# Performance work log

Hardware: AMD Instinct MI355X
Metric: run time of the kernel (lower is better)

Reference implementation:

```python
import jax, jax.numpy as jnp
import numpy as np

UP_RATIO = 2
DOWN_RATIO = 2
K = 12  # hard-coded filter size assumed by the fused kernel


def kaiser_sinc_filter1d(cutoff, half_width, kernel_size):
    # Exact replica of BigVGAN's kaiser_sinc_filter1d (even kernel branch).
    half_size = kernel_size // 2
    delta_f = 4.0 * half_width
    A = 2.285 * (half_size - 1) * np.pi * delta_f + 7.95
    if A > 50.0:
        beta = 0.1102 * (A - 8.7)
    elif A >= 21.0:
        beta = 0.5842 * (A - 21.0) ** 0.4 + 0.07886 * (A - 21.0)
    else:
        beta = 0.0
    window = np.kaiser(kernel_size, beta)  # symmetric, == torch.kaiser_window(periodic=False)
    time = np.arange(-half_size, half_size) + 0.5  # even kernel size
    filt = 2.0 * cutoff * window * np.sinc(2.0 * cutoff * time)
    filt = filt / filt.sum()
    return filt.astype(np.float32)


def setup_inputs() -> dict:
    key = jax.random.key(0)
    k1, k2, k3 = jax.random.split(key, 3)
    B, C, T = 16, 512, 8192
    x = jax.random.normal(k1, (B, C, T), dtype=jnp.float32)
    # log-scale SnakeBeta parameters (alpha_logscale=True -> params stored in log space)
    alpha = jax.random.normal(k2, (C,), dtype=jnp.float32) * 0.1
    beta = jax.random.normal(k3, (C,), dtype=jnp.float32) * 0.1
    up_filter = jnp.asarray(kaiser_sinc_filter1d(0.5 / UP_RATIO, 0.6 / UP_RATIO, K))
    down_filter = jnp.asarray(kaiser_sinc_filter1d(0.5 / DOWN_RATIO, 0.6 / DOWN_RATIO, K))
    return {"x": x, "up_filter": up_filter, "down_filter": down_filter,
            "alpha": alpha, "beta": beta}


def _depthwise_conv(x, filt, stride=1, lhs_dilation=1, pad=(0, 0)):
    # x: (B, C, T); shared 1-tap-bank depthwise conv: fold channels into batch.
    B, C, T = x.shape
    xr = x.reshape(B * C, 1, T)
    w = filt.reshape(1, 1, -1)
    out = jax.lax.conv_general_dilated(
        xr, w, window_strides=(stride,), padding=[pad],
        lhs_dilation=(lhs_dilation,),
        dimension_numbers=("NCH", "OIH", "NCH"))
    return out.reshape(B, C, -1)


def reference(x, up_filter, down_filter, alpha, beta):
    B, C, T = x.shape
    # ---- UpSample1d(ratio=2, kernel_size=12): replicate pad + conv_transpose ----
    pad = K // UP_RATIO - 1                              # 5
    pad_left = pad * UP_RATIO + (K - UP_RATIO) // 2      # 15
    pad_right = pad * UP_RATIO + (K - UP_RATIO + 1) // 2  # 15
    xp = jnp.pad(x, ((0, 0), (0, 0), (pad, pad)), mode="edge")
    # conv_transpose1d(stride=s) == lhs-dilated conv with flipped kernel, full padding
    up = UP_RATIO * _depthwise_conv(xp, up_filter[::-1],
                                    lhs_dilation=UP_RATIO, pad=(K - 1, K - 1))
    up = up[..., pad_left: up.shape[-1] - pad_right]      # (B, C, 2T)
    # ---- SnakeBeta activation (log-scale alpha/beta) ----
    a = jnp.exp(alpha)[None, :, None]
    b = jnp.exp(beta)[None, :, None]
    act = up + (1.0 / (b + 1e-9)) * jnp.sin(up * a) ** 2
    # ---- DownSample1d: replicate-padded lowpass FIR, stride 2 ----
    dl = K // 2 - 1   # 5 (even kernel)
    dr = K // 2       # 6
    actp = jnp.pad(act, ((0, 0), (0, 0), (dl, dr)), mode="edge")
    out = _depthwise_conv(actp, down_filter, stride=DOWN_RATIO)  # (B, C, T)
    return out
```

## Files before the change

### kernel.cpp

```cpp
#include <hip/hip_runtime.h>


#define T_LEN 8192
#define C_CH  512
#define B_N   16
#define W     8
#define BLOCK 256

__global__ __launch_bounds__(BLOCK) void act1d_kernel(
    const float* __restrict__ x,
    const float* __restrict__ uf_g,
    const float* __restrict__ df_g,
    const float* __restrict__ alpha,
    const float* __restrict__ beta,
    float* __restrict__ out)
{
    const int T = T_LEN;
    const int bid = blockIdx.x;
    const int row = bid >> 2;
    const int chunk = bid & 3;
    const int c = row & (C_CH - 1);
    const int nb = chunk * (BLOCK * W) + (int)threadIdx.x * W;
    const long rowoff = (long)row * T;
    const float* xrow = x + rowoff;

    float uf[12], df[12];
#pragma unroll
    for (int k = 0; k < 12; ++k) { uf[k] = 2.0f * uf_g[k]; df[k] = df_g[k]; }

    const float ea   = __expf(alpha[c]);
    const float invb = 1.0f / (__expf(beta[c]) + 1e-9f);

    float a[26];

    const bool interior = (nb >= 8) && (nb + 16 <= T);
    if (interior) {
        float xr[24];
        const float4* xv = (const float4*)(xrow + nb - 8);
#pragma unroll
        for (int k = 0; k < 6; ++k) {
            float4 v = xv[k];
            xr[4*k+0] = v.x; xr[4*k+1] = v.y; xr[4*k+2] = v.z; xr[4*k+3] = v.w;
        }
#pragma unroll
        for (int j = 0; j < 26; ++j) {
            const int xi = ((j - 5) >> 1) + 8;
            float up;
            if ((j & 1) == 0) {
                up = uf[0]*xr[xi+3] + uf[2]*xr[xi+2] + uf[4]*xr[xi+1]
                   + uf[6]*xr[xi]   + uf[8]*xr[xi-1] + uf[10]*xr[xi-2];
            } else {
                up = uf[1]*xr[xi+2] + uf[3]*xr[xi+1] + uf[5]*xr[xi]
                   + uf[7]*xr[xi-1] + uf[9]*xr[xi-2] + uf[11]*xr[xi-3];
            }
            const float sv = __sinf(up * ea);
            a[j] = fmaf(invb * sv, sv, up);
        }
    } else {
#pragma unroll
        for (int j = 0; j < 26; ++j) {
            int t = 2*nb - 5 + j;
            t = min(max(t, 0), 2*T - 1);
            const int s = t >> 1;
            const int par = t & 1;
            float xv7[7];
#pragma unroll
            for (int m = 0; m < 7; ++m) {
                int g = s - 3 + m;
                g = min(max(g, 0), T - 1);
                xv7[m] = xrow[g];
            }
            const float upo = uf[0]*xv7[6] + uf[2]*xv7[5] + uf[4]*xv7[4]
                            + uf[6]*xv7[3] + uf[8]*xv7[2] + uf[10]*xv7[1];
            const float upe = uf[1]*xv7[5] + uf[3]*xv7[4] + uf[5]*xv7[3]
                            + uf[7]*xv7[2] + uf[9]*xv7[1] + uf[11]*xv7[0];
            const float up = par ? upo : upe;
            const float sv = __sinf(up * ea);
            a[j] = fmaf(invb * sv, sv, up);
        }
    }

    float o[W];
#pragma unroll
    for (int d = 0; d < W; ++d) {
        float acc = 0.0f;
#pragma unroll
        for (int k = 0; k < 12; ++k) acc = fmaf(df[k], a[2*d + k], acc);
        o[d] = acc;
    }
    float4* ov = (float4*)(out + rowoff + nb);
    ov[0] = make_float4(o[0], o[1], o[2], o[3]);
    ov[1] = make_float4(o[4], o[5], o[6], o[7]);
}

extern "C" void kernel_launch(void* const* d_in, const int* in_sizes, int n_in,
                              void* d_out, int out_size, void* d_ws, size_t ws_size,
                              hipStream_t stream) {
    const float* x  = (const float*)d_in[0];
    const float* uf = (const float*)d_in[1];
    const float* df = (const float*)d_in[2];
    const float* al = (const float*)d_in[3];
    const float* be = (const float*)d_in[4];
    float* outp = (float*)d_out;

    const int grid = B_N * C_CH * (T_LEN / (BLOCK * W));
    act1d_kernel<<<grid, BLOCK, 0, stream>>>(x, uf, df, al, be, outp);
}
```

Baseline: 468.7 us.

## Double outputs per thread and move boundary handling to a separate edge kernel

Each thread now produces 16 outputs instead of 8. That cuts the overlap recompute of upsampled halo samples, which was 26 activations per 8 outputs and is now 42 per 16. The clamped gather path is removed from the main kernel, which now always does a clamped vector load. A second small kernel overwrites the first and last 16 outputs of each row with correct replicate-padded values. The cost is higher register pressure from the larger arrays and an extra kernel launch, and correctness depends on the edge kernel running after the main one on the same stream.

```diff
diff --git a/kernel.cpp b/kernel.cpp
--- a/kernel.cpp
+++ b/kernel.cpp
@@ -4,10 +4,10 @@
 #define T_LEN 8192
 #define C_CH  512
 #define B_N   16
-#define W     8
+#define W     16
 #define BLOCK 256
 
-__global__ __launch_bounds__(BLOCK) void act1d_kernel(
+__global__ __launch_bounds__(BLOCK) void act1d_main(
     const float* __restrict__ x,
     const float* __restrict__ uf_g,
     const float* __restrict__ df_g,
@@ -17,8 +17,8 @@
 {
     const int T = T_LEN;
     const int bid = blockIdx.x;
-    const int row = bid >> 2;
-    const int chunk = bid & 3;
+    const int row = bid >> 1;
+    const int chunk = bid & 1;
     const int c = row & (C_CH - 1);
     const int nb = chunk * (BLOCK * W) + (int)threadIdx.x * W;
     const long rowoff = (long)row * T;
@@ -31,66 +31,94 @@
     const float ea   = __expf(alpha[c]);
     const float invb = 1.0f / (__expf(beta[c]) + 1e-9f);
 
-    float a[26];
-
-    const bool interior = (nb >= 8) && (nb + 16 <= T);
-    if (interior) {
-        float xr[24];
-        const float4* xv = (const float4*)(xrow + nb - 8);
+    const int base = min(max(nb - 8, 0), T - 32);
+    float xr[32];
+    const float4* xv = (const float4*)(xrow + base);
 #pragma unroll
-        for (int k = 0; k < 6; ++k) {
-            float4 v = xv[k];
-            xr[4*k+0] = v.x; xr[4*k+1] = v.y; xr[4*k+2] = v.z; xr[4*k+3] = v.w;
-        }
-#pragma unroll
-        for (int j = 0; j < 26; ++j) {
-            const int xi = ((j - 5) >> 1) + 8;
-            float up;
-            if ((j & 1) == 0) {
-                up = uf[0]*xr[xi+3] + uf[2]*xr[xi+2] + uf[4]*xr[xi+1]
-                   + uf[6]*xr[xi]   + uf[8]*xr[xi-1] + uf[10]*xr[xi-2];
-            } else {
-                up = uf[1]*xr[xi+2] + uf[3]*xr[xi+1] + uf[5]*xr[xi]
-                   + uf[7]*xr[xi-1] + uf[9]*xr[xi-2] + uf[11]*xr[xi-3];
-            }
-            const float sv = __sinf(up * ea);
-            a[j] = fmaf(invb * sv, sv, up);
-        }
-    } else {
-#pragma unroll
-        for (int j = 0; j < 26; ++j) {
-            int t = 2*nb - 5 + j;
-            t = min(max(t, 0), 2*T - 1);
-            const int s = t >> 1;
-            const int par = t & 1;
-            float xv7[7];
-#pragma unroll
-            for (int m = 0; m < 7; ++m) {
-                int g = s - 3 + m;
-                g = min(max(g, 0), T - 1);
-                xv7[m] = xrow[g];
-            }
-            const float upo = uf[0]*xv7[6] + uf[2]*xv7[5] + uf[4]*xv7[4]
-                            + uf[6]*xv7[3] + uf[8]*xv7[2] + uf[10]*xv7[1];
-            const float upe = uf[1]*xv7[5] + uf[3]*xv7[4] + uf[5]*xv7[3]
-                            + uf[7]*xv7[2] + uf[9]*xv7[1] + uf[11]*xv7[0];
-            const float up = par ? upo : upe;
-            const float sv = __sinf(up * ea);
-            a[j] = fmaf(invb * sv, sv, up);
-        }
+    for (int k = 0; k < 8; ++k) {
+        float4 v = xv[k];
+        xr[4*k+0] = v.x; xr[4*k+1] = v.y; xr[4*k+2] = v.z; xr[4*k+3] = v.w;
     }
 
-    float o[W];
+    float a[42];
 #pragma unroll
-    for (int d = 0; d < W; ++d) {
-        float acc = 0.0f;
+    for (int j = 0; j < 42; ++j) {
+        const int xi = ((j - 5) >> 1) + 8;
+        float up;
+        if ((j & 1) == 0) {
+            up = uf[0]*xr[xi+3] + uf[2]*xr[xi+2] + uf[4]*xr[xi+1]
+               + uf[6]*xr[xi]   + uf[8]*xr[xi-1] + uf[10]*xr[xi-2];
+        } else {
+            up = uf[1]*xr[xi+2] + uf[3]*xr[xi+1] + uf[5]*xr[xi]
+               + uf[7]*xr[xi-1] + uf[9]*xr[xi-2] + uf[11]*xr[xi-3];
+        }
+        const float sv = __sinf(up * ea);
+        a[j] = fmaf(invb * sv, sv, up);
+    }
+
+    float4* ov = (float4*)(out + rowoff + nb);
 #pragma unroll
-        for (int k = 0; k < 12; ++k) acc = fmaf(df[k], a[2*d + k], acc);
-        o[d] = acc;
+    for (int q = 0; q < 4; ++q) {
+        float o[4];
+#pragma unroll
+        for (int dd = 0; dd < 4; ++dd) {
+            const int d = 4*q + dd;
+            float acc = 0.0f;
+#pragma unroll
+            for (int k = 0; k < 12; ++k) acc = fmaf(df[k], a[2*d + k], acc);
+            o[dd] = acc;
+        }
+        ov[q] = make_float4(o[0], o[1], o[2], o[3]);
     }
-    float4* ov = (float4*)(out + rowoff + nb);
-    ov[0] = make_float4(o[0], o[1], o[2], o[3]);
-    ov[1] = make_float4(o[4], o[5], o[6], o[7]);
+}
+
+__global__ __launch_bounds__(64) void act1d_edge(
+    const float* __restrict__ x,
+    const float* __restrict__ uf_g,
+    const float* __restrict__ df_g,
+    const float* __restrict__ alpha,
+    const float* __restrict__ beta,
+    float* __restrict__ out)
+{
+    const int T = T_LEN;
+    const int row = blockIdx.x;
+    const int i = (int)threadIdx.x;
+    if (i >= 32) return;
+    const int n = (i < 16) ? i : (T - 32 + i);
+    const int c = row & (C_CH - 1);
+    const long rowoff = (long)row * T;
+    const float* xrow = x + rowoff;
+
+    float uf[12], df[12];
+#pragma unroll
+    for (int k = 0; k < 12; ++k) { uf[k] = 2.0f * uf_g[k]; df[k] = df_g[k]; }
+    const float ea   = __expf(alpha[c]);
+    const float invb = 1.0f / (__expf(beta[c]) + 1e-9f);
+
+    float acc = 0.0f;
+#pragma unroll
+    for (int k = 0; k < 12; ++k) {
+        int t = 2*n + k - 5;
+        t = min(max(t, 0), 2*T - 1);
+        const int s = t >> 1;
+        const int par = t & 1;
+        float xv7[7];
+#pragma unroll
+        for (int m = 0; m < 7; ++m) {
+            int g = s - 3 + m;
+            g = min(max(g, 0), T - 1);
+            xv7[m] = xrow[g];
+        }
+        const float upo = uf[0]*xv7[6] + uf[2]*xv7[5] + uf[4]*xv7[4]
+                        + uf[6]*xv7[3] + uf[8]*xv7[2] + uf[10]*xv7[1];
+        const float upe = uf[1]*xv7[5] + uf[3]*xv7[4] + uf[5]*xv7[3]
+                        + uf[7]*xv7[2] + uf[9]*xv7[1] + uf[11]*xv7[0];
+        const float up = par ? upo : upe;
+        const float sv = __sinf(up * ea);
+        const float av = fmaf(invb * sv, sv, up);
+        acc = fmaf(df[k], av, acc);
+    }
+    out[rowoff + n] = acc;
 }
 
 extern "C" void kernel_launch(void* const* d_in, const int* in_sizes, int n_in,
@@ -103,6 +131,8 @@
     const float* be = (const float*)d_in[4];
     float* outp = (float*)d_out;
 
-    const int grid = B_N * C_CH * (T_LEN / (BLOCK * W));
-    act1d_kernel<<<grid, BLOCK, 0, stream>>>(x, uf, df, al, be, outp);
+    const int rows = B_N * C_CH;
+    const int grid = rows * (T_LEN / (BLOCK * W));
+    act1d_main<<<grid, BLOCK, 0, stream>>>(x, uf, df, al, be, outp);
+    act1d_edge<<<rows, 64, 0, stream>>>(x, uf, df, al, be, outp);
 }
```

New measurement: 504.0 us. +7.5%, slower.
